# Kernel tuning notes

Measured on AMD Instinct MI355X. Metric: run time of the kernel, lower is better.

## Reference

```python
import jax, jax.numpy as jnp
import numpy as np

EPS = 1e-9

def setup_inputs() -> dict:
    key = jax.random.key(0)
    k_x, k_eo, k_r, k_w, k_u = jax.random.split(key, 5)
    B, T, D, E, K = 4, 2048, 1024, 8, 2
    x = jax.random.normal(k_x, (B, T, D), dtype=jnp.float32)
    expert_outputs = jax.random.normal(k_eo, (E, B, T, D), dtype=jnp.float32)
    rewards = jax.random.normal(k_r, (B, T), dtype=jnp.float32)
    W = jax.random.normal(k_w, (D, E), dtype=jnp.float32) / np.sqrt(D).astype(np.float32)
    b = jnp.zeros((E,), dtype=jnp.float32)
    baseline_value = jnp.zeros((), dtype=jnp.float32)
    noise_u = jax.random.uniform(k_u, (B, T, E), dtype=jnp.float32)
    return {"x": x, "expert_outputs": expert_outputs, "rewards": rewards,
            "W": W, "b": b, "baseline_value": baseline_value,
            "noise_u": noise_u, "top_k": K}

def reference(x, expert_outputs, rewards, W, b, baseline_value, noise_u, top_k):
    # Gate logits + softmax: [B,T,E]
    logits = jnp.einsum('btd,de->bte', x, W) + b
    probs = jax.nn.softmax(logits, axis=-1)
    log_probs = jnp.log(probs + EPS)
    # multinomial-without-replacement == Gumbel top-k on log probs
    u = noise_u * (1.0 - 2e-7) + 1e-7  # keep strictly in (0,1)
    gumbel = -jnp.log(-jnp.log(u))
    _, expert_indices = jax.lax.top_k(log_probs + gumbel, top_k)  # [B,T,K] int32
    # Combine: single indexed gather instead of masked K*E loop (same math)
    eo = jnp.transpose(expert_outputs, (1, 2, 0, 3))  # [B,T,E,D]
    gathered = jnp.take_along_axis(eo, expert_indices[..., None], axis=2)  # [B,T,K,D]
    final_output = gathered.sum(axis=2) / top_k  # [B,T,D]
    # REINFORCE aux loss
    selected_log_probs = jnp.take_along_axis(log_probs, expert_indices, axis=-1).sum(axis=-1)  # [B,T]
    advantage = jax.lax.stop_gradient(rewards - baseline_value)
    aux_loss = -jnp.mean(advantage * selected_log_probs)
    return final_output, aux_loss
```

## Files before the change

kernel.cpp:

```cpp
#include <hip/hip_runtime.h>


#define GATE_EPS 1e-9f

__global__ __launch_bounds__(256) void rlgate_fused(
    const float* __restrict__ x,
    const float* __restrict__ eo,
    const float* __restrict__ rewards,
    const float* __restrict__ W,
    const float* __restrict__ bvec,
    const float* __restrict__ baseline,
    const float* __restrict__ noise,
    float* __restrict__ out,
    float* __restrict__ aux_ws,
    int BT, int D)
{
    constexpr int E = 8;
    const int bt   = blockIdx.x;
    const int tid  = threadIdx.x;
    const int lane = tid & 63;
    const int wave = tid >> 6;

    const float4 xv = ((const float4*)(x + (size_t)bt * D))[tid];
    const float xs[4] = {xv.x, xv.y, xv.z, xv.w};
    float part[E];
#pragma unroll
    for (int e = 0; e < E; ++e) part[e] = 0.0f;
    const float* wr = W + (size_t)(tid * 4) * E;
#pragma unroll
    for (int j = 0; j < 4; ++j) {
#pragma unroll
        for (int e = 0; e < E; ++e)
            part[e] = fmaf(xs[j], wr[j * E + e], part[e]);
    }
#pragma unroll
    for (int off = 32; off > 0; off >>= 1) {
#pragma unroll
        for (int e = 0; e < E; ++e)
            part[e] += __shfl_xor(part[e], off, 64);
    }

    __shared__ float red[4][E];
    __shared__ int   sh_idx[2];
    if (lane == 0) {
#pragma unroll
        for (int e = 0; e < E; ++e) red[wave][e] = part[e];
    }
    __syncthreads();

    if (tid == 0) {
        const float c_scale = (float)(1.0 - 2e-7);
        const float c_shift = (float)(1e-7);

        float lg[E], lp[E], sc[E];
        float m = -INFINITY;
#pragma unroll
        for (int e = 0; e < E; ++e) {
            lg[e] = red[0][e] + red[1][e] + red[2][e] + red[3][e] + bvec[e];
            m = fmaxf(m, lg[e]);
        }
        float s = 0.0f;
        float ex[E];
#pragma unroll
        for (int e = 0; e < E; ++e) { ex[e] = expf(lg[e] - m); s += ex[e]; }
#pragma unroll
        for (int e = 0; e < E; ++e) {
            float p = ex[e] / s;
            lp[e]   = logf(p + GATE_EPS);
            float u = noise[(size_t)bt * E + e] * c_scale + c_shift;
            float g = -logf(-logf(u));
            sc[e]   = lp[e] + g;
        }
        int i1 = 0; float s1 = sc[0];
#pragma unroll
        for (int e = 1; e < E; ++e) if (sc[e] > s1) { s1 = sc[e]; i1 = e; }
        int i2 = -1; float s2 = -INFINITY;
#pragma unroll
        for (int e = 0; e < E; ++e)
            if (e != i1 && sc[e] > s2) { s2 = sc[e]; i2 = e; }

        sh_idx[0] = i1;
        sh_idx[1] = i2;
        aux_ws[bt] = (rewards[bt] - baseline[0]) * (lp[i1] + lp[i2]);
    }
    __syncthreads();

    const size_t b1 = ((size_t)sh_idx[0] * BT + bt) * (size_t)D;
    const size_t b2 = ((size_t)sh_idx[1] * BT + bt) * (size_t)D;
    const float4 a = ((const float4*)(eo + b1))[tid];
    const float4 c = ((const float4*)(eo + b2))[tid];
    float4 o;
    o.x = (a.x + c.x) * 0.5f;
    o.y = (a.y + c.y) * 0.5f;
    o.z = (a.z + c.z) * 0.5f;
    o.w = (a.w + c.w) * 0.5f;
    ((float4*)(out + (size_t)bt * D))[tid] = o;
}

__global__ __launch_bounds__(256) void rlgate_aux_reduce(
    const float* __restrict__ aux_ws, float* __restrict__ out_aux, int BT)
{
    const int tid  = threadIdx.x;
    const int lane = tid & 63;
    const int wave = tid >> 6;
    float s = 0.0f;
    for (int i = tid; i < BT; i += 256) s += aux_ws[i];
#pragma unroll
    for (int off = 32; off > 0; off >>= 1) s += __shfl_xor(s, off, 64);
    __shared__ float red[4];
    if (lane == 0) red[wave] = s;
    __syncthreads();
    if (tid == 0)
        out_aux[0] = -(red[0] + red[1] + red[2] + red[3]) / (float)BT;
}

extern "C" void kernel_launch(void* const* d_in, const int* in_sizes, int n_in,
                              void* d_out, int out_size, void* d_ws, size_t ws_size,
                              hipStream_t stream)
{
    const float* x        = (const float*)d_in[0];
    const float* eo       = (const float*)d_in[1];
    const float* rewards  = (const float*)d_in[2];
    const float* W        = (const float*)d_in[3];
    const float* bvec     = (const float*)d_in[4];
    const float* baseline = (const float*)d_in[5];
    const float* noise    = (const float*)d_in[6];

    const int BT = in_sizes[2];
    const int D  = in_sizes[0] / BT;

    float* out    = (float*)d_out;
    float* outaux = out + (size_t)BT * D;
    float* aux_ws = (float*)d_ws;

    rlgate_fused<<<BT, D / 4, 0, stream>>>(x, eo, rewards, W, bvec, baseline,
                                           noise, out, aux_ws, BT, D);
    rlgate_aux_reduce<<<1, 256, 0, stream>>>(aux_ws, outaux, BT);
}
```

Baseline: 374.4 us.

## Split gating and expert combine into separate kernels with LDS-staged gate weights

New measurement: 383.9 us. +2.5%, slower.

```diff
diff --git a/kernel.cpp b/kernel.cpp
--- a/kernel.cpp
+++ b/kernel.cpp
@@ -3,98 +3,121 @@
 
 #define GATE_EPS 1e-9f
 
-__global__ __launch_bounds__(256) void rlgate_fused(
+__global__ __launch_bounds__(256) void rlgate_gate(
     const float* __restrict__ x,
-    const float* __restrict__ eo,
     const float* __restrict__ rewards,
     const float* __restrict__ W,
     const float* __restrict__ bvec,
     const float* __restrict__ baseline,
     const float* __restrict__ noise,
-    float* __restrict__ out,
+    int2*  __restrict__ idx_ws,
     float* __restrict__ aux_ws,
     int BT, int D)
 {
     constexpr int E = 8;
-    const int bt   = blockIdx.x;
     const int tid  = threadIdx.x;
     const int lane = tid & 63;
     const int wave = tid >> 6;
 
-    const float4 xv = ((const float4*)(x + (size_t)bt * D))[tid];
-    const float xs[4] = {xv.x, xv.y, xv.z, xv.w};
-    float part[E];
+    __shared__ float WT[E][1024];
 #pragma unroll
-    for (int e = 0; e < E; ++e) part[e] = 0.0f;
-    const float* wr = W + (size_t)(tid * 4) * E;
-#pragma unroll
-    for (int j = 0; j < 4; ++j) {
-#pragma unroll
-        for (int e = 0; e < E; ++e)
-            part[e] = fmaf(xs[j], wr[j * E + e], part[e]);
-    }
-#pragma unroll
-    for (int off = 32; off > 0; off >>= 1) {
-#pragma unroll
-        for (int e = 0; e < E; ++e)
-            part[e] += __shfl_xor(part[e], off, 64);
-    }
-
-    __shared__ float red[4][E];
-    __shared__ int   sh_idx[2];
-    if (lane == 0) {
-#pragma unroll
-        for (int e = 0; e < E; ++e) red[wave][e] = part[e];
+    for (int k = 0; k < 4; ++k) {
+        const int r = tid + 256 * k;
+        const float4 w0 = ((const float4*)W)[r * 2];
+        const float4 w1 = ((const float4*)W)[r * 2 + 1];
+        WT[0][r] = w0.x; WT[1][r] = w0.y; WT[2][r] = w0.z; WT[3][r] = w0.w;
+        WT[4][r] = w1.x; WT[5][r] = w1.y; WT[6][r] = w1.z; WT[7][r] = w1.w;
     }
     __syncthreads();
 
-    if (tid == 0) {
-        const float c_scale = (float)(1.0 - 2e-7);
-        const float c_shift = (float)(1e-7);
+    for (int it = 0; it < 4; ++it) {
+        const int tk = blockIdx.x * 16 + wave * 4 + it;
 
-        float lg[E], lp[E], sc[E];
-        float m = -INFINITY;
+        float part[4][E];
 #pragma unroll
-        for (int e = 0; e < E; ++e) {
-            lg[e] = red[0][e] + red[1][e] + red[2][e] + red[3][e] + bvec[e];
-            m = fmaxf(m, lg[e]);
+        for (int c = 0; c < 4; ++c)
+#pragma unroll
+            for (int e = 0; e < E; ++e) part[c][e] = 0.0f;
+
+#pragma unroll
+        for (int c = 0; c < 4; ++c) {
+            const float4 xv = ((const float4*)(x + (size_t)tk * D))[c * 64 + lane];
+            const float xs[4] = {xv.x, xv.y, xv.z, xv.w};
+            const int r0 = (c * 64 + lane) * 4;
+#pragma unroll
+            for (int e = 0; e < E; ++e) {
+                const float4 wv = *(const float4*)(&WT[e][r0]);
+                float a = part[c][e];
+                a = fmaf(xs[0], wv.x, a);
+                a = fmaf(xs[1], wv.y, a);
+                a = fmaf(xs[2], wv.z, a);
+                a = fmaf(xs[3], wv.w, a);
+                part[c][e] = a;
+            }
         }
-        float s = 0.0f;
-        float ex[E];
 #pragma unroll
-        for (int e = 0; e < E; ++e) { ex[e] = expf(lg[e] - m); s += ex[e]; }
+        for (int off = 32; off > 0; off >>= 1) {
 #pragma unroll
-        for (int e = 0; e < E; ++e) {
-            float p = ex[e] / s;
-            lp[e]   = logf(p + GATE_EPS);
-            float u = noise[(size_t)bt * E + e] * c_scale + c_shift;
-            float g = -logf(-logf(u));
-            sc[e]   = lp[e] + g;
+            for (int c = 0; c < 4; ++c)
+#pragma unroll
+                for (int e = 0; e < E; ++e)
+                    part[c][e] += __shfl_xor(part[c][e], off, 64);
         }
-        int i1 = 0; float s1 = sc[0];
+
+        if (lane == 0) {
+            const float c_scale = (float)(1.0 - 2e-7);
+            const float c_shift = (float)(1e-7);
+
+            float lg[E], lp[E], sc[E];
+            float m = -INFINITY;
 #pragma unroll
-        for (int e = 1; e < E; ++e) if (sc[e] > s1) { s1 = sc[e]; i1 = e; }
-        int i2 = -1; float s2 = -INFINITY;
+            for (int e = 0; e < E; ++e) {
+                lg[e] = part[0][e] + part[1][e] + part[2][e] + part[3][e] + bvec[e];
+                m = fmaxf(m, lg[e]);
+            }
+            float s = 0.0f;
+            float ex[E];
 #pragma unroll
-        for (int e = 0; e < E; ++e)
-            if (e != i1 && sc[e] > s2) { s2 = sc[e]; i2 = e; }
+            for (int e = 0; e < E; ++e) { ex[e] = expf(lg[e] - m); s += ex[e]; }
+#pragma unroll
+            for (int e = 0; e < E; ++e) {
+                float p = ex[e] / s;
+                lp[e]   = logf(p + GATE_EPS);
+                float u = noise[(size_t)tk * E + e] * c_scale + c_shift;
+                float g = -logf(-logf(u));
+                sc[e]   = lp[e] + g;
+            }
+            int i1 = 0; float s1 = sc[0];
+#pragma unroll
+            for (int e = 1; e < E; ++e) if (sc[e] > s1) { s1 = sc[e]; i1 = e; }
+            int i2 = -1; float s2 = -INFINITY;
+#pragma unroll
+            for (int e = 0; e < E; ++e)
+                if (e != i1 && sc[e] > s2) { s2 = sc[e]; i2 = e; }
 
-        sh_idx[0] = i1;
-        sh_idx[1] = i2;
-        aux_ws[bt] = (rewards[bt] - baseline[0]) * (lp[i1] + lp[i2]);
+            idx_ws[tk] = make_int2(i1, i2);
+            aux_ws[tk] = (rewards[tk] - baseline[0]) * (lp[i1] + lp[i2]);
+        }
     }
-    __syncthreads();
+}
 
-    const size_t b1 = ((size_t)sh_idx[0] * BT + bt) * (size_t)D;
-    const size_t b2 = ((size_t)sh_idx[1] * BT + bt) * (size_t)D;
-    const float4 a = ((const float4*)(eo + b1))[tid];
-    const float4 c = ((const float4*)(eo + b2))[tid];
+__global__ __launch_bounds__(256) void rlgate_combine(
+    const float* __restrict__ eo,
+    const int2*  __restrict__ idx_ws,
+    float* __restrict__ out,
+    int BT, int D)
+{
+    const int bt  = blockIdx.x;
+    const int tid = threadIdx.x;
+    const int2 id = idx_ws[bt];
+    const float4 a = ((const float4*)(eo + ((size_t)id.x * BT + bt) * (size_t)D))[tid];
+    const float4 b = ((const float4*)(eo + ((size_t)id.y * BT + bt) * (size_t)D))[tid];
     float4 o;
-    o.x = (a.x + c.x) * 0.5f;
-    o.y = (a.y + c.y) * 0.5f;
-    o.z = (a.z + c.z) * 0.5f;
-    o.w = (a.w + c.w) * 0.5f;
-    ((float4*)(out + (size_t)bt * D))[tid] = o;
+    o.x = (a.x + b.x) * 0.5f;
+    o.y = (a.y + b.y) * 0.5f;
+    o.z = (a.z + b.z) * 0.5f;
+    o.w = (a.w + b.w) * 0.5f;
+    ((float4*)(out + (size_t)bt * (size_t)D))[tid] = o;
 }
 
 __global__ __launch_bounds__(256) void rlgate_aux_reduce(
@@ -132,8 +155,10 @@
     float* out    = (float*)d_out;
     float* outaux = out + (size_t)BT * D;
     float* aux_ws = (float*)d_ws;
+    int2*  idx_ws = (int2*)((char*)d_ws + (size_t)BT * sizeof(float));
 
-    rlgate_fused<<<BT, D / 4, 0, stream>>>(x, eo, rewards, W, bvec, baseline,
-                                           noise, out, aux_ws, BT, D);
+    rlgate_gate<<<BT / 16, 256, 0, stream>>>(x, rewards, W, bvec, baseline,
+                                             noise, idx_ws, aux_ws, BT, D);
+    rlgate_combine<<<BT, D / 4, 0, stream>>>(eo, idx_ws, out, BT, D);
     rlgate_aux_reduce<<<1, 256, 0, stream>>>(aux_ws, outaux, BT);
 }
```
